# Optimization experiments

Measured on AMD Instinct MI355X. Metric: run time of the kernel, lower is better.

## Reference

```python
import jax, jax.numpy as jnp
import numpy as np
import math

VOCAB, D_MODEL, IN_DIM, OUT_DIM, BLOCK = 50257, 256, 64, 64, 2048

def setup_inputs() -> dict:
    key = jax.random.key(0)
    ks = jax.random.split(key, 8)
    B, S = 4, 1024
    x = jax.random.normal(ks[0], (B, S, IN_DIM), dtype=jnp.float32)
    embedding = jax.random.normal(ks[1], (VOCAB, D_MODEL), dtype=jnp.float32)
    wpe = 0.01 * jax.random.normal(ks[2], (BLOCK, D_MODEL), dtype=jnp.float32)
    lim_e = 1.0 / math.sqrt(IN_DIM)
    enc_w = jax.random.uniform(ks[3], (D_MODEL, IN_DIM), minval=-lim_e, maxval=lim_e, dtype=jnp.float32)
    enc_b = jax.random.uniform(ks[4], (D_MODEL,), minval=-lim_e, maxval=lim_e, dtype=jnp.float32)
    ln_g = jnp.ones((D_MODEL,), dtype=jnp.float32)
    ln_b = jnp.zeros((D_MODEL,), dtype=jnp.float32)
    lim_d = 1.0 / math.sqrt(D_MODEL)
    dec_w = jax.random.uniform(ks[5], (OUT_DIM, D_MODEL), minval=-lim_d, maxval=lim_d, dtype=jnp.float32)
    dec_b = jax.random.uniform(ks[6], (OUT_DIM,), minval=-lim_d, maxval=lim_d, dtype=jnp.float32)
    return {"x": x, "embedding": embedding, "wpe": wpe, "enc_w": enc_w, "enc_b": enc_b,
            "ln_g": ln_g, "ln_b": ln_b, "dec_w": dec_w, "dec_b": dec_b}

def _layernorm(h, g, b, eps=1e-5):
    mu = jnp.mean(h, axis=-1, keepdims=True)
    var = jnp.var(h, axis=-1, keepdims=True)
    return (h - mu) * jax.lax.rsqrt(var + eps) * g + b

def reference(x, embedding, wpe, enc_w, enc_b, ln_g, ln_b, dec_w, dec_b):
    B, S, _ = x.shape
    pos_emb = wpe[:S]                                  # [S, D]
    h = jnp.einsum('bsi,di->bsd', x, enc_w) + enc_b    # encoder
    h = h + pos_emb
    h = _layernorm(h, ln_g, ln_b)
    logits = jnp.einsum('bsd,vd->bsv', h, embedding) / math.sqrt(D_MODEL)
    probs = jax.nn.softmax(logits, axis=-1)            # [B, S, V]
    quantize = jnp.einsum('bsv,vd->bsd', probs, embedding)
    out = jnp.einsum('bsd,od->bso', quantize, dec_w) + dec_b
    return (out, jnp.argmax(probs, axis=-1))
```

## Files before the change

### kernel.cpp

```cpp
#include <hip/hip_runtime.h>
#include <math.h>

#define VOCAB   50257
#define VP64    50304
#define NT64    786
#define NVT     1571
#define DM      256
#define INDIM   64
#define OUTDIM  64
#define NROWS   4096
#define SEQ     1024
#define NSLICE  8
#define NTT     64
#define MARGIN  5e-3f
#define FLAGCAP 1024
#define EP      264
#define FOFF    4.0f

typedef _Float16 f16;
typedef _Float16 half8 __attribute__((ext_vector_type(8)));
typedef _Float16 half4v __attribute__((ext_vector_type(4)));
typedef float floatx4 __attribute__((ext_vector_type(4)));
typedef float f32x16 __attribute__((ext_vector_type(16)));

static __device__ __forceinline__ unsigned ldsaddr(const void* p)
{
    return (unsigned)(unsigned long long)(__attribute__((address_space(3))) const void*)p;
}

template <int IMM>
static __device__ __forceinline__ void trrd(unsigned a, half4v& d)
{
    asm volatile("ds_read_b64_tr_b16 %0, %1 offset:%2"
                 : "=v"(d) : "v"(a), "i"(IMM));
}

__global__ __launch_bounds__(256) void encode_ln_kernel(
    const float* __restrict__ x, const float* __restrict__ enc_w,
    const float* __restrict__ enc_b, const float* __restrict__ wpe,
    const float* __restrict__ ln_g, const float* __restrict__ ln_b,
    float* __restrict__ hs_out, f16* __restrict__ q_hi, f16* __restrict__ q_lo,
    int* flagcnt, int write_q)
{
    const int row = blockIdx.x;
    const int s   = row & (SEQ - 1);
    const int d   = threadIdx.x;

    __shared__ float xs[INDIM];
    __shared__ float w1[4], w2[4];

    if (d < INDIM) xs[d] = x[(size_t)row * INDIM + d];
    __syncthreads();

    const float4* wrow = (const float4*)(enc_w + (size_t)d * INDIM);
    float dot = 0.f;
#pragma unroll
    for (int i = 0; i < INDIM / 4; ++i) {
        float4 w4 = wrow[i];
        dot += w4.x * xs[i * 4 + 0] + w4.y * xs[i * 4 + 1]
             + w4.z * xs[i * 4 + 2] + w4.w * xs[i * 4 + 3];
    }
    float h = dot + enc_b[d] + wpe[(size_t)s * DM + d];

    float v1 = h, v2 = h * h;
#pragma unroll
    for (int mask = 1; mask < 64; mask <<= 1) {
        v1 += __shfl_xor(v1, mask, 64);
        v2 += __shfl_xor(v2, mask, 64);
    }
    if ((d & 63) == 0) { w1[d >> 6] = v1; w2[d >> 6] = v2; }
    __syncthreads();
    float S1 = w1[0] + w1[1] + w1[2] + w1[3];
    float S2 = w2[0] + w2[1] + w2[2] + w2[3];
    float mu  = S1 * (1.f / DM);
    float var = S2 * (1.f / DM) - mu * mu;
    float rs  = rsqrtf(var + 1e-5f);
    float hn  = (h - mu) * rs * ln_g[d] + ln_b[d];
    float hsv = hn * 0.0625f;
    hs_out[(size_t)row * DM + d] = hsv;
    if (write_q) {
        f16 hi = (f16)hsv;
        q_hi[(size_t)row * DM + d] = hi;
        q_lo[(size_t)row * DM + d] = (f16)(hsv - (float)hi);
    }
    if (row == 0 && d == 0 && write_q) *flagcnt = 0;
}

__global__ __launch_bounds__(256) void prep_emb(
    const float* __restrict__ emb, f16* __restrict__ e_hi)
{
    const size_t i = ((size_t)blockIdx.x * 256 + threadIdx.x) * 8;
    if (i >= (size_t)VP64 * DM) return;
    const size_t v = i >> 8;
    half8 h;
    if (v < VOCAB) {
        const float* src = emb + i;
        float4 f0 = *(const float4*)(src);
        float4 f1 = *(const float4*)(src + 4);
        h[0]=(f16)f0.x; h[1]=(f16)f0.y; h[2]=(f16)f0.z; h[3]=(f16)f0.w;
        h[4]=(f16)f1.x; h[5]=(f16)f1.y; h[6]=(f16)f1.z; h[7]=(f16)f1.w;
    } else {
#pragma unroll
        for (int j = 0; j < 8; ++j) h[j] = (f16)0.f;
    }
    *(half8*)(e_hi + i) = h;
}

__global__ __launch_bounds__(256, 2) void fused_main(
    const f16* __restrict__ e_hi, const f16* __restrict__ q_hi,
    float* __restrict__ pO, float* __restrict__ pm1, float* __restrict__ pm2,
    float* __restrict__ pl, int* __restrict__ pi1)
{
    const int tid  = threadIdx.x;
    const int wave = tid >> 6;
    const int lane = tid & 63;
    const int l31  = lane & 31;
    const int h    = lane >> 5;
    const int thalf = wave & 1;
    const int vhalf = wave >> 1;
    const int slice = blockIdx.x & 7;
    const int tt    = blockIdx.x >> 3;

    __shared__ f16 ehi_s[2][64 * DM];
    __shared__ f16 plds[64][72];
    __shared__ float mmrg[2][32][3];
    __shared__ int   imrg[2][32];

    half8 qf[16];
    {
        const f16* qb = q_hi + ((size_t)(tt * 64 + thalf * 32 + l31)) * DM + h * 8;
#pragma unroll
        for (int s = 0; s < 16; ++s) qf[s] = *(const half8*)(qb + s * 16);
    }

    f32x16 O0, O1, O2, O3;
#pragma unroll
    for (int i = 0; i < 16; ++i) { O0[i]=0.f; O1[i]=0.f; O2[i]=0.f; O3[i]=0.f; }
    float t1a = -INFINITY, t2a = -INFINITY, la_a = 0.f;
    float t1b = -INFINITY, t2b = -INFINITY, la_b = 0.f;
    int tia = 0, tib = 0;

    const int ntile = (NT64 - slice + NSLICE - 1) / NSLICE;

    const int aoff = (vhalf * 8 + (l31 >> 2)) * 1024 + (l31 & 3) * 16 + h * 8;

    const unsigned trbase = ldsaddr(&ehi_s[0][0]) +
        (unsigned)(vhalf * 1024 + h * 4096 + ((lane >> 4) & 1) * 128 + (lane & 15) * 2);

    const int lan3 = lane >> 3;
    const int lv   = (lane & 7) >> 1;
    const int ld8  = (lane & 1) * 8;

#define STAGE_TILE(BB, V0)                                                   \
    {                                                                        \
        _Pragma("unroll")                                                    \
        for (int c_ = 0; c_ < 8; ++c_) {                                     \
            const int sub_ = wave * 64 + c_ * 8 + lan3;                      \
            const int v4_ = sub_ >> 4, d16_ = sub_ & 15;                     \
            const f16* src_ = e_hi + (size_t)((V0) + v4_ * 4 + lv) * DM      \
                              + d16_ * 16 + ld8;                             \
            f16* dst_ = &ehi_s[(BB)][wave * 4096 + c_ * 512];                \
            __builtin_amdgcn_global_load_lds(                                \
                (const __attribute__((address_space(1))) void*)src_,         \
                (__attribute__((address_space(3))) void*)dst_, 16, 0, 0);    \
        }                                                                    \
    }

#define G2STEP(DL, OV)                                                         \
    {                                                                          \
        half4v u00, u01, u10, u11, u20, u21, u30, u31;                         \
        trrd<(DL)*256 +     0>(tb, u00);                                       \
        trrd<(DL)*256 +  2048>(tb, u01);                                       \
        trrd<(DL)*256 +  8192>(tb, u10);                                       \
        trrd<(DL)*256 + 10240>(tb, u11);                                       \
        trrd<(DL)*256 + 16384>(tb, u20);                                       \
        trrd<(DL)*256 + 18432>(tb, u21);                                       \
        trrd<(DL)*256 + 24576>(tb, u30);                                       \
        trrd<(DL)*256 + 26624>(tb, u31);                                       \
        __asm__ volatile("s_waitcnt lgkmcnt(0)" ::: "memory");                 \
        __builtin_amdgcn_sched_barrier(0);                                     \
        __builtin_amdgcn_s_setprio(1);                                         \
        OV = __builtin_amdgcn_mfma_f32_32x32x16_f16(pa0,                       \
                 __builtin_shufflevector(u00, u01, 0,1,2,3,4,5,6,7), OV,0,0,0);\
        OV = __builtin_amdgcn_mfma_f32_32x32x16_f16(pa1,                       \
                 __builtin_shufflevector(u10, u11, 0,1,2,3,4,5,6,7), OV,0,0,0);\
        OV = __builtin_amdgcn_mfma_f32_32x32x16_f16(pa2,                       \
                 __builtin_shufflevector(u20, u21, 0,1,2,3,4,5,6,7), OV,0,0,0);\
        OV = __builtin_amdgcn_mfma_f32_32x32x16_f16(pa3,                       \
                 __builtin_shufflevector(u30, u31, 0,1,2,3,4,5,6,7), OV,0,0,0);\
        __builtin_amdgcn_s_setprio(0);                                         \
    }

    STAGE_TILE(0, slice * 64);
    __syncthreads();

    for (int it = 0; it < ntile; ++it) {
        const int b  = it & 1;
        const int v0 = (slice + it * NSLICE) * 64;
        const bool pre = (it + 1 < ntile);

        f32x16 C;
#pragma unroll
        for (int i = 0; i < 16; ++i) C[i] = 0.f;
        {
            const f16* ab = &ehi_s[b][aoff];
            __builtin_amdgcn_s_setprio(1);
#pragma unroll
            for (int s = 0; s < 16; ++s)
                C = __builtin_amdgcn_mfma_f32_32x32x16_f16(
                        *(const half8*)(ab + s * 64), qf[s], C, 0, 0, 0);
            __builtin_amdgcn_s_setprio(0);
        }

        if (v0 + 64 > VOCAB) {
#pragma unroll
            for (int r = 0; r < 16; ++r) {
                int v = v0 + vhalf * 32 + (r & 3) + 8 * (r >> 2) + 4 * h;
                if (v >= VOCAB) C[r] = -INFINITY;
            }
        }

        {
            f16* prow = &plds[thalf * 32 + l31][vhalf * 32 + h * 4];
#pragma unroll
            for (int g2 = 0; g2 < 4; ++g2) {
                half4v hv;
#pragma unroll
                for (int j = 0; j < 4; ++j) {
                    float e = __expf(C[g2 * 4 + j] - FOFF);
                    hv[j] = (f16)e;
                    if (g2 < 2) la_a += e; else la_b += e;
                }
                *(half4v*)(prow + g2 * 8) = hv;
            }
        }
#pragma unroll
        for (int r = 0; r < 8; ++r) {
            float sv = C[r];
            int vg = v0 + vhalf * 32 + (r & 3) + 8 * (r >> 2) + 4 * h;
            t2a = fmaxf(t2a, fminf(t1a, sv));
            tia = (sv > t1a) ? vg : tia;
            t1a = fmaxf(t1a, sv);
        }
#pragma unroll
        for (int r = 8; r < 16; ++r) {
            float sv = C[r];
            int vg = v0 + vhalf * 32 + (r & 3) + 8 * (r >> 2) + 4 * h;
            t2b = fmaxf(t2b, fminf(t1b, sv));
            tib = (sv > t1b) ? vg : tib;
            t1b = fmaxf(t1b, sv);
        }

        __syncthreads();

        if (pre) STAGE_TILE(b ^ 1, v0 + NSLICE * 64);

        {
            const f16* pb = &plds[thalf * 32 + l31][h * 8];
            half8 pa0 = *(const half8*)(pb);
            half8 pa1 = *(const half8*)(pb + 16);
            half8 pa2 = *(const half8*)(pb + 32);
            half8 pa3 = *(const half8*)(pb + 48);
            const unsigned tb = trbase + (unsigned)(b * 32768);
            G2STEP(0, O0)
            G2STEP(1, O1)
            G2STEP(2, O2)
            G2STEP(3, O3)
        }

        __syncthreads();
    }
#undef STAGE_TILE
#undef G2STEP

    {
        float* ob = pO + ((size_t)slice * NROWS + tt * 64 + thalf * 32) * DM + vhalf * 128;
#pragma unroll
        for (int r = 0; r < 16; ++r) {
            const size_t rb = (size_t)((r & 3) + 8 * (r >> 2) + 4 * h) * DM + l31;
            ob[rb +  0] = O0[r];
            ob[rb + 32] = O1[r];
            ob[rb + 64] = O2[r];
            ob[rb + 96] = O3[r];
        }
    }

    float nt1 = fmaxf(t1a, t1b);
    float nt2 = fmaxf(fminf(t1a, t1b), fmaxf(t2a, t2b));
    int   nti = (t1b > t1a) ? tib : tia;
    float nl  = la_a + la_b;
    {
        float o1 = __shfl_xor(nt1, 32);
        float o2 = __shfl_xor(nt2, 32);
        int   oi = __shfl_xor(nti, 32);
        float ol = __shfl_xor(nl, 32);
        nt2 = fmaxf(fminf(nt1, o1), fmaxf(nt2, o2));
        nti = (o1 > nt1) ? oi : nti;
        nt1 = fmaxf(nt1, o1);
        nl += ol;
    }
    if (vhalf == 1 && h == 0) {
        mmrg[thalf][l31][0] = nt1;
        mmrg[thalf][l31][1] = nt2;
        mmrg[thalf][l31][2] = nl;
        imrg[thalf][l31] = nti;
    }
    __syncthreads();
    if (vhalf == 0 && h == 0) {
        float o1 = mmrg[thalf][l31][0];
        float o2 = mmrg[thalf][l31][1];
        float ol = mmrg[thalf][l31][2];
        int   oi = imrg[thalf][l31];
        nt2 = fmaxf(fminf(nt1, o1), fmaxf(nt2, o2));
        nti = (o1 > nt1) ? oi : nti;
        nt1 = fmaxf(nt1, o1);
        nl += ol;
        const int idx = slice * NROWS + tt * 64 + thalf * 32 + l31;
        pm1[idx] = nt1;
        pm2[idx] = nt2;
        pl [idx] = nl;
        pi1[idx] = nti;
    }
}

__global__ __launch_bounds__(256) void merge_decode(
    const float* __restrict__ pO, const float* __restrict__ pm1,
    const float* __restrict__ pm2, const float* __restrict__ pl,
    const int* __restrict__ pi1,
    const float* __restrict__ dec_w, const float* __restrict__ dec_b,
    float* __restrict__ out, float* __restrict__ amax_out,
    unsigned long long* __restrict__ amax64, int* flagcnt, int* flaglist,
    int* __restrict__ flbyte)
{
    const int tt  = blockIdx.x;
    const int tid = threadIdx.x;
    __shared__ float q_s[16][DM];
    __shared__ float lI[16];

    if (tid < 16) {
        const int row = tt * 16 + tid;
        float M = -INFINITY, M2 = -INFINITY; int win = 0;
        float lt = 0.f;
        for (int s = 0; s < NSLICE; ++s) {
            float v = pm1[s * NROWS + row];
            if (v > M) { M2 = M; M = v; win = s; }
            else M2 = fmaxf(M2, v);
            M2 = fmaxf(M2, pm2[s * NROWS + row]);
            lt += pl[s * NROWS + row];
        }
        amax_out[row] = (float)pi1[win * NROWS + row];
        amax64[row] = 0ull;
        int fl = (M - M2) < MARGIN;
        flbyte[row] = fl;
        if (fl) {
            int pos = atomicAdd(flagcnt, 1);
            if (pos < FLAGCAP) flaglist[pos] = row;
        }
        lI[tid] = 1.f / lt;
    }
    __syncthreads();
    {
        const int m = tid >> 4, d0 = (tid & 15) * 16;
        const int row = tt * 16 + m;
        float4 acc[4];
#pragma unroll
        for (int k = 0; k < 4; ++k) acc[k] = make_float4(0.f, 0.f, 0.f, 0.f);
        for (int s = 0; s < NSLICE; ++s) {
            const float4* pp = (const float4*)(pO + ((size_t)s * NROWS + row) * DM + d0);
#pragma unroll
            for (int k = 0; k < 4; ++k) {
                float4 v = pp[k];
                acc[k].x += v.x; acc[k].y += v.y;
                acc[k].z += v.z; acc[k].w += v.w;
            }
        }
        const float li = lI[m];
#pragma unroll
        for (int k = 0; k < 4; ++k) {
            acc[k].x *= li; acc[k].y *= li; acc[k].z *= li; acc[k].w *= li;
            *(float4*)&q_s[m][d0 + k * 4] = acc[k];
        }
    }
    __syncthreads();
    {
        const int o = tid & 63;
        const float4* wp = (const float4*)(dec_w + (size_t)o * DM);
#pragma unroll
        for (int k = 0; k < 4; ++k) {
            const int m = (tid >> 6) + k * 4;
            const float4* qp = (const float4*)&q_s[m][0];
            float acc = 0.f;
            for (int d4 = 0; d4 < DM / 4; ++d4) {
                float4 w = wp[d4], q = qp[d4];
                acc += w.x * q.x + w.y * q.y + w.z * q.z + w.w * q.w;
            }
            out[(size_t)(tt * 16 + m) * OUTDIM + o] = acc + dec_b[o];
        }
    }
}

__global__ __launch_bounds__(256) void gather_flagged(
    const f16* __restrict__ q_hi, const f16* __restrict__ q_lo,
    const int* __restrict__ flagcnt, const int* __restrict__ flaglist,
    f16* __restrict__ qg)
{
    int cnt = *flagcnt; if (cnt > FLAGCAP) cnt = FLAGCAP;
    const int j = blockIdx.x;
    if (j >= cnt) return;
    const int row = flaglist[j];
    const int t = threadIdx.x;
    qg[(size_t)j * 512 + t]       = q_hi[(size_t)row * DM + t];
    qg[(size_t)j * 512 + 256 + t] = q_lo[(size_t)row * DM + t];
}

__global__ __launch_bounds__(64) void recheck_rows(
    const float* __restrict__ emb, const f16* __restrict__ qg,
    const int* __restrict__ flagcnt, const int* __restrict__ flaglist,
    unsigned long long* __restrict__ amax64)
{
    int cnt = *flagcnt; if (cnt > FLAGCAP) cnt = FLAGCAP;
    if (cnt == 0) return;
    const int v0   = blockIdx.x * 32;
    const int lane = threadIdx.x;
    const int m_   = lane & 15;
    const int quad = lane >> 4;

    __shared__ f16 ehi[32][EP];
    __shared__ f16 elo[32][EP];

    for (int i = 0; i < 32; ++i) {
        const int v = v0 + i;
        float4 f = (v < VOCAB) ? *(const float4*)(emb + (size_t)v * DM + lane * 4)
                               : make_float4(0.f, 0.f, 0.f, 0.f);
        half4v hh, hl;
        hh[0]=(f16)f.x; hh[1]=(f16)f.y; hh[2]=(f16)f.z; hh[3]=(f16)f.w;
        hl[0]=(f16)(f.x-(float)hh[0]); hl[1]=(f16)(f.y-(float)hh[1]);
        hl[2]=(f16)(f.z-(float)hh[2]); hl[3]=(f16)(f.w-(float)hh[3]);
        *(half4v*)&ehi[i][lane * 4] = hh;
        *(half4v*)&elo[i][lane * 4] = hl;
    }
    __asm__ volatile("s_waitcnt lgkmcnt(0)" ::: "memory");

    for (int c0 = 0; c0 < cnt; c0 += 16) {
        const bool haveb = (c0 + m_) < cnt;
        const int fidx = haveb ? (c0 + m_) : 0;

        half8 bh[8], bl[8];
        const f16* qb = qg + (size_t)fidx * 512 + quad * 8;
#pragma unroll
        for (int s = 0; s < 8; ++s) {
            bh[s] = *(const half8*)(qb + s * 32);
            bl[s] = *(const half8*)(qb + 256 + s * 32);
        }

        floatx4 C0, C1;
        C0[0]=0.f; C0[1]=0.f; C0[2]=0.f; C0[3]=0.f;
        C1[0]=0.f; C1[1]=0.f; C1[2]=0.f; C1[3]=0.f;
#pragma unroll
        for (int s = 0; s < 8; ++s) {
            half8 ah0 = *(const half8*)&ehi[m_][quad * 8 + 32 * s];
            half8 al0 = *(const half8*)&elo[m_][quad * 8 + 32 * s];
            half8 ah1 = *(const half8*)&ehi[m_ + 16][quad * 8 + 32 * s];
            half8 al1 = *(const half8*)&elo[m_ + 16][quad * 8 + 32 * s];
            C0 = __builtin_amdgcn_mfma_f32_16x16x32_f16(ah0, bh[s], C0, 0, 0, 0);
            C0 = __builtin_amdgcn_mfma_f32_16x16x32_f16(ah0, bl[s], C0, 0, 0, 0);
            C0 = __builtin_amdgcn_mfma_f32_16x16x32_f16(al0, bh[s], C0, 0, 0, 0);
            C0 = __builtin_amdgcn_mfma_f32_16x16x32_f16(al0, bl[s], C0, 0, 0, 0);
            C1 = __builtin_amdgcn_mfma_f32_16x16x32_f16(ah1, bh[s], C1, 0, 0, 0);
            C1 = __builtin_amdgcn_mfma_f32_16x16x32_f16(ah1, bl[s], C1, 0, 0, 0);
            C1 = __builtin_amdgcn_mfma_f32_16x16x32_f16(al1, bh[s], C1, 0, 0, 0);
            C1 = __builtin_amdgcn_mfma_f32_16x16x32_f16(al1, bl[s], C1, 0, 0, 0);
        }

        float bv = -INFINITY; int bi = 0;
#pragma unroll
        for (int r = 0; r < 4; ++r) {
            int v = v0 + quad * 4 + r;
            float val = (v < VOCAB) ? C0[r] : -INFINITY;
            if (val > bv) { bv = val; bi = v; }
            int v2 = v + 16;
            float val2 = (v2 < VOCAB) ? C1[r] : -INFINITY;
            if (val2 > bv) { bv = val2; bi = v2; }
        }
#pragma unroll
        for (int offc = 16; offc <= 32; offc += 16) {
            float ov = __shfl_xor(bv, offc);
            int   oi = __shfl_xor(bi, offc);
            if (ov > bv || (ov == bv && oi < bi)) { bv = ov; bi = oi; }
        }
        if (quad == 0 && haveb) {
            unsigned u = __float_as_uint(bv);
            u = (u & 0x80000000u) ? ~u : (u | 0x80000000u);
            unsigned long long key =
                ((unsigned long long)u << 32) | (unsigned)(~bi);
            atomicMax(&amax64[flaglist[fidx]], key);
        }
    }
}

__global__ void finalize_amax(const int* __restrict__ flbyte,
                              const unsigned long long* __restrict__ amax64,
                              float* __restrict__ amax_out)
{
    int row = blockIdx.x * 256 + threadIdx.x;
    if (row >= NROWS) return;
    if (flbyte[row]) {
        unsigned long long u = amax64[row];
        if (u) {
            unsigned idx = ~(unsigned)(u & 0xffffffffu);
            amax_out[row] = (float)idx;
        }
    }
}

#define RPB 4
__global__ __launch_bounds__(256, 2) void fused_softmax_quant_kernel(
    const float* __restrict__ emb, const float* __restrict__ hs,
    const float* __restrict__ dec_w, const float* __restrict__ dec_b,
    float* __restrict__ out, float* __restrict__ amax_out)
{
    const int tid  = threadIdx.x;
    const int g    = tid >> 4;
    const int q    = tid & 15;
    const int row0 = blockIdx.x * RPB;

    __shared__ __align__(16) float q_lds[RPB][DM];
    __shared__ float sm[16][RPB], sl[16][RPB];
    __shared__ int   sam[16][RPB];
    __shared__ float sLf[RPB];

    for (int i = tid; i < RPB * DM; i += 256) (&q_lds[0][0])[i] = 0.f;

    float4 hsr[RPB][4];
#pragma unroll
    for (int r = 0; r < RPB; ++r)
#pragma unroll
        for (int o = 0; o < 4; ++o)
            hsr[r][o] = *(const float4*)(hs + (size_t)(row0 + r) * DM + o * 64 + q * 4);

    float m[RPB], l[RPB];
    int   am[RPB];
    float4 acc[RPB][4];
#pragma unroll
    for (int r = 0; r < RPB; ++r) {
        m[r] = -INFINITY; l[r] = 0.f; am[r] = 0;
#pragma unroll
        for (int o = 0; o < 4; ++o) acc[r][o] = make_float4(0.f, 0.f, 0.f, 0.f);
    }

    float ecur[16], enxt[16];
    {
        size_t b0 = (size_t)g * DM + q * 4;
#pragma unroll
        for (int o = 0; o < 4; ++o)
            *(float4*)(enxt + o * 4) = *(const float4*)(emb + b0 + o * 64);
    }

#pragma unroll 1
    for (int v = g; v < VOCAB; v += 16) {
#pragma unroll
        for (int j = 0; j < 16; ++j) ecur[j] = enxt[j];
        int vn = (v + 16 < VOCAB) ? v + 16 : v;
        size_t bn = (size_t)vn * DM + q * 4;
#pragma unroll
        for (int o = 0; o < 4; ++o)
            *(float4*)(enxt + o * 4) = *(const float4*)(emb + bn + o * 64);

        float part[RPB];
#pragma unroll
        for (int r = 0; r < RPB; ++r) {
            const float* hp = (const float*)&hsr[r][0];
            float t = 0.f;
#pragma unroll
            for (int j = 0; j < 16; ++j) t += ecur[j] * hp[j];
            part[r] = t;
        }
#pragma unroll
        for (int mask = 8; mask >= 1; mask >>= 1)
#pragma unroll
            for (int r = 0; r < RPB; ++r)
                part[r] += __shfl_xor(part[r], mask, 16);

#pragma unroll
        for (int r = 0; r < RPB; ++r) {
            float lg = part[r];
            float* ap = (float*)&acc[r][0];
            if (lg > m[r]) {
                float c = __expf(m[r] - lg);
                m[r] = lg; am[r] = v;
                l[r] = l[r] * c + 1.f;
#pragma unroll
                for (int j = 0; j < 16; ++j) ap[j] = ap[j] * c + ecur[j];
            } else {
                float p = __expf(lg - m[r]);
                l[r] += p;
#pragma unroll
                for (int j = 0; j < 16; ++j) ap[j] += p * ecur[j];
            }
        }
    }

    if (q == 0) {
#pragma unroll
        for (int r = 0; r < RPB; ++r) { sm[g][r] = m[r]; sl[g][r] = l[r]; sam[g][r] = am[r]; }
    }
    __syncthreads();

    float wgt[RPB], Lr[RPB];
    int   A[RPB];
#pragma unroll
    for (int r = 0; r < RPB; ++r) {
        float M = -INFINITY; int a = 0;
        for (int gg = 0; gg < 16; ++gg) {
            float mv = sm[gg][r];
            if (mv > M) { M = mv; a = sam[gg][r]; }
        }
        float L = 0.f;
        for (int gg = 0; gg < 16; ++gg) L += sl[gg][r] * __expf(sm[gg][r] - M);
        wgt[r] = __expf(m[r] - M);
        Lr[r] = L; A[r] = a;
    }

#pragma unroll
    for (int r = 0; r < RPB; ++r) {
        const float* ap = (const float*)&acc[r][0];
#pragma unroll
        for (int j = 0; j < 16; ++j) {
            float vs = ap[j] * wgt[r];
            vs += __shfl_xor(vs, 16, 64);
            vs += __shfl_xor(vs, 32, 64);
            if ((g & 3) == 0) {
                int o = j >> 2, c = j & 3;
                atomicAdd(&q_lds[r][o * 64 + q * 4 + c], vs);
            }
        }
    }
    if (tid == 0) {
#pragma unroll
        for (int r = 0; r < RPB; ++r) {
            sLf[r] = Lr[r];
            amax_out[row0 + r] = (float)A[r];
        }
    }
    __syncthreads();

    {
        const int r = tid >> 6, o = tid & 63;
        const float4* dwp = (const float4*)(dec_w + (size_t)o * DM);
        const float4* qp  = (const float4*)&q_lds[r][0];
        float s = 0.f;
#pragma unroll 8
        for (int d4 = 0; d4 < DM / 4; ++d4) {
            float4 wv = dwp[d4];
            float4 qv = qp[d4];
            s += wv.x * qv.x + wv.y * qv.y + wv.z * qv.z + wv.w * qv.w;
        }
        s = s / sLf[r] + dec_b[o];
        out[(size_t)(row0 + r) * OUTDIM + o] = s;
    }
}

extern "C" void kernel_launch(void* const* d_in, const int* in_sizes, int n_in,
                              void* d_out, int out_size, void* d_ws, size_t ws_size,
                              hipStream_t stream)
{
    const float* x     = (const float*)d_in[0];
    const float* emb   = (const float*)d_in[1];
    const float* wpe   = (const float*)d_in[2];
    const float* enc_w = (const float*)d_in[3];
    const float* enc_b = (const float*)d_in[4];
    const float* ln_g  = (const float*)d_in[5];
    const float* ln_b  = (const float*)d_in[6];
    const float* dec_w = (const float*)d_in[7];
    const float* dec_b = (const float*)d_in[8];

    float* out      = (float*)d_out;
    float* amax_out = out + (size_t)NROWS * OUTDIM;

    char* w = (char*)d_ws;
    size_t off = 0;
    float* hs = (float*)(w + off);          off += (size_t)NROWS * DM * 4;
    f16* q_hi = (f16*)(w + off);            off += (size_t)NROWS * DM * 2;
    f16* q_lo = (f16*)(w + off);            off += (size_t)NROWS * DM * 2;
    f16* e_hi = (f16*)(w + off);            off += (size_t)VP64 * DM * 2;
    float* pO = (float*)(w + off);          off += (size_t)NSLICE * NROWS * DM * 4;
    float* pm1 = (float*)(w + off);         off += (size_t)NSLICE * NROWS * 4;
    float* pm2 = (float*)(w + off);         off += (size_t)NSLICE * NROWS * 4;
    float* pl  = (float*)(w + off);         off += (size_t)NSLICE * NROWS * 4;
    int*   pi1 = (int*)(w + off);           off += (size_t)NSLICE * NROWS * 4;
    unsigned long long* amax64 = (unsigned long long*)(w + off); off += (size_t)NROWS * 8;
    int* flagcnt  = (int*)(w + off);        off += 256;
    int* flaglist = (int*)(w + off);        off += FLAGCAP * 4;
    int* flbyte   = (int*)(w + off);        off += (size_t)NROWS * 4;
    f16* qg       = (f16*)(w + off);        off += (size_t)FLAGCAP * 512 * 2;

    const bool full = (ws_size >= off);

    encode_ln_kernel<<<NROWS, 256, 0, stream>>>(x, enc_w, enc_b, wpe, ln_g, ln_b,
                                                hs, q_hi, q_lo, flagcnt, full ? 1 : 0);
    if (full) {
        prep_emb<<<((size_t)VP64 * DM) / (256 * 8), 256, 0, stream>>>(emb, e_hi);
        fused_main<<<NTT * NSLICE, 256, 0, stream>>>(e_hi, q_hi,
                                                     pO, pm1, pm2, pl, pi1);
        merge_decode<<<NROWS / 16, 256, 0, stream>>>(pO, pm1, pm2, pl, pi1, dec_w, dec_b,
                                                     out, amax_out, amax64, flagcnt,
                                                     flaglist, flbyte);
        gather_flagged<<<FLAGCAP, 256, 0, stream>>>(q_hi, q_lo, flagcnt, flaglist, qg);
        recheck_rows<<<NVT, 64, 0, stream>>>(emb, qg, flagcnt, flaglist, amax64);
        finalize_amax<<<(NROWS + 255) / 256, 256, 0, stream>>>(flbyte, amax64, amax_out);
    } else {
        fused_softmax_quant_kernel<<<NROWS / RPB, 256, 0, stream>>>(emb, hs, dec_w,
                                                                    dec_b, out, amax_out);
    }
}
```

Measured before the change: 526.1 us.

## Keep softmax probabilities in registers via permlane swap, split PV by vocab half

Removes the plds shared-memory round trip for the exp'd probability tile: probabilities are packed to fp16 and rearranged across lane halves with v_permlane32_swap so each wave feeds its own 32-vocab slice directly into the PV MFMAs. Each wave now accumulates all 256 output dims over its vocab half (8 accumulators instead of 4), and the two vocab halves are reduced through LDS at the end. The next-tile prefetch is issued at the start of the iteration, and one __syncthreads per tile is dropped. In exchange it doubles accumulator register pressure (128 more VGPRs/AGPRs), which may hurt occupancy at launch_bounds(256,2), and it adds a final LDS reduction.

```diff
diff --git a/kernel.cpp b/kernel.cpp
--- a/kernel.cpp
+++ b/kernel.cpp
@@ -122,7 +122,6 @@
     const int tt    = blockIdx.x >> 3;
 
     __shared__ f16 ehi_s[2][64 * DM];
-    __shared__ f16 plds[64][72];
     __shared__ float mmrg[2][32][3];
     __shared__ int   imrg[2][32];
 
@@ -133,9 +132,12 @@
         for (int s = 0; s < 16; ++s) qf[s] = *(const half8*)(qb + s * 16);
     }
 
-    f32x16 O0, O1, O2, O3;
-#pragma unroll
-    for (int i = 0; i < 16; ++i) { O0[i]=0.f; O1[i]=0.f; O2[i]=0.f; O3[i]=0.f; }
+    f32x16 O0, O1, O2, O3, O4, O5, O6, O7;
+#pragma unroll
+    for (int i = 0; i < 16; ++i) {
+        O0[i]=0.f; O1[i]=0.f; O2[i]=0.f; O3[i]=0.f;
+        O4[i]=0.f; O5[i]=0.f; O6[i]=0.f; O7[i]=0.f;
+    }
     float t1a = -INFINITY, t2a = -INFINITY, la_a = 0.f;
     float t1b = -INFINITY, t2b = -INFINITY, la_b = 0.f;
     int tia = 0, tib = 0;
@@ -145,7 +147,7 @@
     const int aoff = (vhalf * 8 + (l31 >> 2)) * 1024 + (l31 & 3) * 16 + h * 8;
 
     const unsigned trbase = ldsaddr(&ehi_s[0][0]) +
-        (unsigned)(vhalf * 1024 + h * 4096 + ((lane >> 4) & 1) * 128 + (lane & 15) * 2);
+        (unsigned)(vhalf * 16384 + h * 4096 + ((lane >> 4) & 1) * 128 + (lane & 15) * 2);
 
     const int lan3 = lane >> 3;
     const int lv   = (lane & 7) >> 1;
@@ -166,28 +168,28 @@
         }                                                                    \
     }
 
-#define G2STEP(DL, OV)                                                         \
+#define G2PAIR(D, OA, OB)                                                      \
     {                                                                          \
-        half4v u00, u01, u10, u11, u20, u21, u30, u31;                         \
-        trrd<(DL)*256 +     0>(tb, u00);                                       \
-        trrd<(DL)*256 +  2048>(tb, u01);                                       \
-        trrd<(DL)*256 +  8192>(tb, u10);                                       \
-        trrd<(DL)*256 + 10240>(tb, u11);                                       \
-        trrd<(DL)*256 + 16384>(tb, u20);                                       \
-        trrd<(DL)*256 + 18432>(tb, u21);                                       \
-        trrd<(DL)*256 + 24576>(tb, u30);                                       \
-        trrd<(DL)*256 + 26624>(tb, u31);                                       \
+        half4v t00, t01, t10, t11, t20, t21, t30, t31;                         \
+        trrd<(D)*256 +     0>(tb, t00);                                        \
+        trrd<(D)*256 +  2048>(tb, t01);                                        \
+        trrd<(D)*256 +  8192>(tb, t10);                                        \
+        trrd<(D)*256 + 10240>(tb, t11);                                        \
+        trrd<(D)*256 +   256>(tb, t20);                                        \
+        trrd<(D)*256 +  2304>(tb, t21);                                        \
+        trrd<(D)*256 +  8448>(tb, t30);                                        \
+        trrd<(D)*256 + 10496>(tb, t31);                                        \
         __asm__ volatile("s_waitcnt lgkmcnt(0)" ::: "memory");                 \
         __builtin_amdgcn_sched_barrier(0);                                     \
         __builtin_amdgcn_s_setprio(1);                                         \
-        OV = __builtin_amdgcn_mfma_f32_32x32x16_f16(pa0,                       \
-                 __builtin_shufflevector(u00, u01, 0,1,2,3,4,5,6,7), OV,0,0,0);\
-        OV = __builtin_amdgcn_mfma_f32_32x32x16_f16(pa1,                       \
-                 __builtin_shufflevector(u10, u11, 0,1,2,3,4,5,6,7), OV,0,0,0);\
-        OV = __builtin_amdgcn_mfma_f32_32x32x16_f16(pa2,                       \
-                 __builtin_shufflevector(u20, u21, 0,1,2,3,4,5,6,7), OV,0,0,0);\
-        OV = __builtin_amdgcn_mfma_f32_32x32x16_f16(pa3,                       \
-                 __builtin_shufflevector(u30, u31, 0,1,2,3,4,5,6,7), OV,0,0,0);\
+        OA = __builtin_amdgcn_mfma_f32_32x32x16_f16(pa0,                       \
+                 __builtin_shufflevector(t00, t01, 0,1,2,3,4,5,6,7), OA,0,0,0);\
+        OA = __builtin_amdgcn_mfma_f32_32x32x16_f16(pa1,                       \
+                 __builtin_shufflevector(t10, t11, 0,1,2,3,4,5,6,7), OA,0,0,0);\
+        OB = __builtin_amdgcn_mfma_f32_32x32x16_f16(pa0,                       \
+                 __builtin_shufflevector(t20, t21, 0,1,2,3,4,5,6,7), OB,0,0,0);\
+        OB = __builtin_amdgcn_mfma_f32_32x32x16_f16(pa1,                       \
+                 __builtin_shufflevector(t30, t31, 0,1,2,3,4,5,6,7), OB,0,0,0);\
         __builtin_amdgcn_s_setprio(0);                                         \
     }
 
@@ -199,6 +201,8 @@
         const int v0 = (slice + it * NSLICE) * 64;
         const bool pre = (it + 1 < ntile);
 
+        if (pre) STAGE_TILE(b ^ 1, v0 + NSLICE * 64);
+
         f32x16 C;
 #pragma unroll
         for (int i = 0; i < 16; ++i) C[i] = 0.f;
@@ -220,20 +224,6 @@
             }
         }
 
-        {
-            f16* prow = &plds[thalf * 32 + l31][vhalf * 32 + h * 4];
-#pragma unroll
-            for (int g2 = 0; g2 < 4; ++g2) {
-                half4v hv;
-#pragma unroll
-                for (int j = 0; j < 4; ++j) {
-                    float e = __expf(C[g2 * 4 + j] - FOFF);
-                    hv[j] = (f16)e;
-                    if (g2 < 2) la_a += e; else la_b += e;
-                }
-                *(half4v*)(prow + g2 * 8) = hv;
-            }
-        }
 #pragma unroll
         for (int r = 0; r < 8; ++r) {
             float sv = C[r];
@@ -251,37 +241,71 @@
             t1b = fmaxf(t1b, sv);
         }
 
+        unsigned Wv[8], Av[8], Bv[8];
+#pragma unroll
+        for (int k = 0; k < 8; ++k) {
+            float e0 = __expf(C[2 * k]     - FOFF);
+            float e1 = __expf(C[2 * k + 1] - FOFF);
+            if (k < 4) la_a += e0 + e1; else la_b += e0 + e1;
+            union { f16 x[2]; unsigned u; } cv;
+            cv.x[0] = (f16)e0; cv.x[1] = (f16)e1;
+            unsigned pa_ = cv.u, pb_ = cv.u;
+            __asm__ volatile("v_permlane32_swap_b32 %0, %1" : "+v"(pa_), "+v"(pb_));
+            Wv[k] = cv.u; Av[k] = pa_; Bv[k] = pb_;
+        }
+        union { unsigned u[4]; half8 v; } up0, up1;
+        up0.u[0] = h ? Bv[2] : Wv[0];
+        up0.u[1] = h ? Bv[3] : Wv[1];
+        up0.u[2] = h ? Wv[2] : Av[0];
+        up0.u[3] = h ? Wv[3] : Av[1];
+        up1.u[0] = h ? Bv[6] : Wv[4];
+        up1.u[1] = h ? Bv[7] : Wv[5];
+        up1.u[2] = h ? Wv[6] : Av[4];
+        up1.u[3] = h ? Wv[7] : Av[5];
+        const half8 pa0 = up0.v, pa1 = up1.v;
+
+        {
+            const unsigned tb = trbase + (unsigned)(b * 32768);
+            G2PAIR(0, O0, O1)
+            G2PAIR(2, O2, O3)
+            G2PAIR(4, O4, O5)
+            G2PAIR(6, O6, O7)
+        }
+
         __syncthreads();
-
-        if (pre) STAGE_TILE(b ^ 1, v0 + NSLICE * 64);
-
-        {
-            const f16* pb = &plds[thalf * 32 + l31][h * 8];
-            half8 pa0 = *(const half8*)(pb);
-            half8 pa1 = *(const half8*)(pb + 16);
-            half8 pa2 = *(const half8*)(pb + 32);
-            half8 pa3 = *(const half8*)(pb + 48);
-            const unsigned tb = trbase + (unsigned)(b * 32768);
-            G2STEP(0, O0)
-            G2STEP(1, O1)
-            G2STEP(2, O2)
-            G2STEP(3, O3)
-        }
-
+    }
+#undef STAGE_TILE
+#undef G2PAIR
+
+    {
+        float* cmb = (float*)&ehi_s[0][0];
+        if (vhalf == 1) {
+            float* dst = cmb + thalf * 8192;
+#pragma unroll
+            for (int r = 0; r < 16; ++r) {
+                float* dr = dst + ((r & 3) + 8 * (r >> 2) + 4 * h) * 256 + l31;
+                dr[0]   = O0[r]; dr[32]  = O1[r]; dr[64]  = O2[r]; dr[96]  = O3[r];
+                dr[128] = O4[r]; dr[160] = O5[r]; dr[192] = O6[r]; dr[224] = O7[r];
+            }
+        }
         __syncthreads();
-    }
-#undef STAGE_TILE
-#undef G2STEP
-
-    {
-        float* ob = pO + ((size_t)slice * NROWS + tt * 64 + thalf * 32) * DM + vhalf * 128;
-#pragma unroll
-        for (int r = 0; r < 16; ++r) {
-            const size_t rb = (size_t)((r & 3) + 8 * (r >> 2) + 4 * h) * DM + l31;
-            ob[rb +  0] = O0[r];
-            ob[rb + 32] = O1[r];
-            ob[rb + 64] = O2[r];
-            ob[rb + 96] = O3[r];
+        if (vhalf == 0) {
+            const float* src = cmb + thalf * 8192;
+            float* ob = pO + ((size_t)slice * NROWS + tt * 64 + thalf * 32) * DM;
+#pragma unroll
+            for (int r = 0; r < 16; ++r) {
+                const int row = (r & 3) + 8 * (r >> 2) + 4 * h;
+                const float* sr = src + row * 256 + l31;
+                float* orow = ob + (size_t)row * DM + l31;
+                orow[0]   = O0[r] + sr[0];
+                orow[32]  = O1[r] + sr[32];
+                orow[64]  = O2[r] + sr[64];
+                orow[96]  = O3[r] + sr[96];
+                orow[128] = O4[r] + sr[128];
+                orow[160] = O5[r] + sr[160];
+                orow[192] = O6[r] + sr[192];
+                orow[224] = O7[r] + sr[224];
+            }
         }
     }
 
```

New measurement: 568.0 us. 8.0% more time.
